# Optimization experiments

Measured on AMD Instinct MI355X. Metric: run time of the kernel, lower is better.

The kernel has to match this reference:

```python
import math
import jax, jax.numpy as jnp
import numpy as np

N_NODES = 100000
N_EDGES = 1600000
IN_DIM = 512
HID = 128
OUT_DIM = 1
N_LAYERS = 8
ALPHA = 0.1
THETA = 0.5


def setup_inputs() -> dict:
    key = jax.random.key(0)
    ks = jax.random.split(key, 8)
    x = jax.random.normal(ks[0], (N_NODES, IN_DIM), dtype=jnp.float32)
    edge_index = jax.random.randint(ks[1], (2, N_EDGES), 0, N_NODES, dtype=jnp.int64)
    edge_weight = jax.random.uniform(ks[2], (N_EDGES,), dtype=jnp.float32)
    s_in = 1.0 / math.sqrt(IN_DIM)
    s_h = 1.0 / math.sqrt(HID)
    W_in = jax.random.uniform(ks[3], (IN_DIM, HID), jnp.float32, -s_in, s_in)
    b_in = jax.random.uniform(ks[4], (HID,), jnp.float32, -s_in, s_in)
    W_layers = jax.random.uniform(ks[5], (N_LAYERS, HID, HID), jnp.float32, -s_h, s_h)
    W_out = jax.random.uniform(ks[6], (HID, OUT_DIM), jnp.float32, -s_h, s_h)
    b_out = jax.random.uniform(ks[7], (OUT_DIM,), jnp.float32, -s_h, s_h)
    return {"x": x, "edge_index": edge_index, "edge_weight": edge_weight,
            "W_in": W_in, "b_in": b_in, "W_layers": W_layers,
            "W_out": W_out, "b_out": b_out}


def _gcn_norm(edge_index, n_nodes, dtype):
    # gcn_norm with add_self_loops=True and unit edge weights
    # (GCN2Net never forwards edge_weight into GCN2Conv).
    loop = jnp.arange(n_nodes, dtype=edge_index.dtype)
    src = jnp.concatenate([edge_index[0], loop])
    dst = jnp.concatenate([edge_index[1], loop])
    w = jnp.ones(src.shape[0], dtype=dtype)
    deg = jax.ops.segment_sum(w, dst, num_segments=n_nodes)
    dinv = jnp.where(deg > 0, jax.lax.rsqrt(deg), 0.0).astype(dtype)
    norm = dinv[src] * w * dinv[dst]
    return src, dst, norm


def reference(x, edge_index, edge_weight, W_in, b_in, W_layers, W_out, b_out):
    n = x.shape[0]
    src, dst, norm = _gcn_norm(edge_index, n, x.dtype)

    x = x @ W_in + b_in          # initial_proj: [N, HID]
    x0 = x
    for i in range(N_LAYERS):
        # sparse neighbor aggregation: A_hat @ x
        agg = jax.ops.segment_sum(x[src] * norm[:, None], dst, num_segments=n)
        # initial residual
        h = (1.0 - ALPHA) * agg + ALPHA * x0
        # identity mapping (shared_weights=True): (1-beta)*h + beta*(h @ W)
        beta = math.log(THETA / (i + 1) + 1.0)
        x = (1.0 - beta) * h + beta * (h @ W_layers[i])
        x = jax.nn.relu(x)
        # dropout omitted (eval mode / drop_prob=0)
    return x @ W_out + b_out     # final_proj: [N, OUT_DIM]
```

## Files before the change

### kernel.cpp

```cpp
#include <hip/hip_runtime.h>
#include <math.h>

#define NN 100000
#define NE 1600000
#define IN_DIM 512
#define HID 128
#define N_LAYERS 8
#define NB 98
#define PADMAX 2000000
#define NBUCK 391
#define BCAP2 4608
#define EPB 4096

typedef __attribute__((ext_vector_type(4))) float f32x4;
typedef __attribute__((ext_vector_type(8))) _Float16 h16x8;
typedef __attribute__((ext_vector_type(2))) _Float16 h16x2;


__global__ __launch_bounds__(256) void bucket2_kernel(
    const int* __restrict__ src, const int* __restrict__ dst,
    int* __restrict__ deg, int* __restrict__ bcnt, int2* __restrict__ pairs) {
    __shared__ int hist[NBUCK];
    __shared__ int scan_[NBUCK + 1];
    __shared__ int gb[NBUCK];
    __shared__ int curs[NBUCK];
    __shared__ int2 lp[EPB];
    int t = threadIdx.x;
    int e0 = blockIdx.x * EPB;
    int ne = NE - e0; if (ne > EPB) ne = EPB;

    for (int i = t; i < NBUCK; i += 256) hist[i] = 0;
    __syncthreads();
    for (int i = t; i < ne; i += 256) {
        int d = dst[e0 + i];
        atomicAdd(&hist[d >> 8], 1);
        atomicAdd(&deg[d], 1);
    }
    __syncthreads();

    if (t < 64) {
        int run = 0;
        for (int c = 0; c < 7; ++c) {
            int i = c * 64 + t;
            int h = (i < NBUCK) ? hist[i] : 0;
            int v = h;
            for (int off = 1; off < 64; off <<= 1) {
                int tmp = __shfl_up(v, off, 64);
                if (t >= off) v += tmp;
            }
            if (i < NBUCK) scan_[i] = run + v - h;
            run += __shfl(v, 63, 64);
        }
        if (t == 0) scan_[NBUCK] = run;
    }
    __syncthreads();

    for (int i = t; i < NBUCK; i += 256) {
        int h = hist[i];
        gb[i] = h ? atomicAdd(&bcnt[i], h) : 0;
        curs[i] = scan_[i];
    }
    __syncthreads();

    for (int i = t; i < ne; i += 256) {
        int d = dst[e0 + i], s = src[e0 + i];
        int slot = atomicAdd(&curs[d >> 8], 1);
        lp[slot] = make_int2(s, d);
    }
    __syncthreads();

    for (int i = t; i < ne; i += 256) {
        int lo = 0, hi = NBUCK;
        while (hi - lo > 1) {
            int mid = (lo + hi) >> 1;
            if (scan_[mid] <= i) lo = mid; else hi = mid;
        }
        pairs[(size_t)lo * BCAP2 + gb[lo] + (i - scan_[lo])] = lp[i];
    }
}

__global__ void scan1_kernel(const int* __restrict__ deg, int* __restrict__ bsum) {
    __shared__ int s[16];
    int gi = blockIdx.x * 1024 + threadIdx.x;
    int d = (gi < NN) ? deg[gi] : 0;
    int r = (d + 3) & ~3;
    for (int off = 32; off; off >>= 1) r += __shfl_down(r, off, 64);
    if ((threadIdx.x & 63) == 0) s[threadIdx.x >> 6] = r;
    __syncthreads();
    if (threadIdx.x == 0) {
        int t = 0;
        for (int i = 0; i < 16; ++i) t += s[i];
        bsum[blockIdx.x] = t;
    }
}

__global__ void scan2_kernel(const int* __restrict__ bsum, int* __restrict__ boff,
                             int* __restrict__ row_ptr,
                             _Float16* __restrict__ sa, _Float16* __restrict__ sb) {
    __shared__ int s[128];
    int tid = threadIdx.x;
    sa[(size_t)NN * HID + tid] = (_Float16)0.f;
    sb[(size_t)NN * HID + tid] = (_Float16)0.f;
    int v = (tid < NB) ? bsum[tid] : 0;
    s[tid] = v;
    __syncthreads();
    for (int off = 1; off < 128; off <<= 1) {
        int t = (tid >= off) ? s[tid - off] : 0;
        __syncthreads();
        s[tid] += t;
        __syncthreads();
    }
    if (tid < NB) boff[tid] = s[tid] - v;
    if (tid == NB - 1) row_ptr[NN] = s[tid];
}

__global__ void scan3_kernel(const int* __restrict__ deg, const int* __restrict__ boff,
                             int* __restrict__ row_ptr, int* __restrict__ cursor,
                             float* __restrict__ dinv) {
    __shared__ int s[1024];
    int tid = threadIdx.x;
    int gi = blockIdx.x * 1024 + tid;
    int d = (gi < NN) ? deg[gi] : 0;
    int v = (d + 3) & ~3;
    s[tid] = v;
    __syncthreads();
    for (int off = 1; off < 1024; off <<= 1) {
        int t = (tid >= off) ? s[tid - off] : 0;
        __syncthreads();
        s[tid] += t;
        __syncthreads();
    }
    if (gi < NN) {
        int o = boff[blockIdx.x] + s[tid] - v;
        row_ptr[gi] = o;
        cursor[gi]  = o;
        dinv[gi]    = rsqrtf((float)(d + 1));
    }
}

__global__ __launch_bounds__(512) void fill2_kernel(
    const int* __restrict__ bcnt, const int2* __restrict__ pairs,
    const int* __restrict__ row_ptr, int* __restrict__ cursor,
    int* __restrict__ col) {
    int b = blockIdx.x;
    int n = bcnt[b];
    const int2* seg = pairs + (size_t)b * BCAP2;
#pragma unroll 4
    for (int i = threadIdx.x; i < n; i += 512) {
        int2 sd = seg[i];
        int pos = atomicAdd(&cursor[sd.y], 1);
        col[pos] = sd.x;
    }
    __syncthreads();
    int d0 = b * 256;
    int d1 = d0 + 256; if (d1 > NN) d1 = NN;
    for (int d = d0 + threadIdx.x; d < d1; d += 512) {
        int rp  = row_ptr[d];
        int end = cursor[d];
        int pend = rp + ((end - rp + 3) & ~3);
        for (int p = end; p < pend; ++p) col[p] = NN;
    }
}


__global__ void wprep_init_kernel(const float* __restrict__ W,
                                  _Float16* __restrict__ Bhi, _Float16* __restrict__ Blo) {
    int t = blockIdx.x * 256 + threadIdx.x;
    if (t >= 8 * 16 * 64) return;
    int lane = t & 63, nkk = t >> 6;
    int n = nkk >> 4, kk = nkk & 15;
    int scol = n * 16 + (lane & 15);
    int sr0 = kk * 32 + (lane >> 4) * 8;
#pragma unroll
    for (int j = 0; j < 8; ++j) {
        float w = W[(size_t)(sr0 + j) * HID + scol];
        _Float16 hi = (_Float16)w;
        _Float16 lo = (_Float16)(w - (float)hi);
        Bhi[(size_t)t * 8 + j] = hi;
        Blo[(size_t)t * 8 + j] = lo;
    }
}

__global__ void wprep_layers_kernel(const float* __restrict__ WL,
                                    _Float16* __restrict__ Bhi, _Float16* __restrict__ Blo) {
    int t = blockIdx.x * 256 + threadIdx.x;
    if (t >= N_LAYERS * 8 * 4 * 64) return;
    int layer = t >> 11;
    int r = t & 2047;
    int lane = r & 63, nkk = r >> 6;
    int n = nkk >> 2, kk = nkk & 3;
    const float* W = WL + (size_t)layer * HID * HID;
    int scol = n * 16 + (lane & 15);
    int sr0 = kk * 32 + (lane >> 4) * 8;
#pragma unroll
    for (int j = 0; j < 8; ++j) {
        float w = W[(size_t)(sr0 + j) * HID + scol];
        _Float16 hi = (_Float16)w;
        _Float16 lo = (_Float16)(w - (float)hi);
        Bhi[(size_t)t * 8 + j] = hi;
        Blo[(size_t)t * 8 + j] = lo;
    }
}


__device__ inline int xsw(int row, int blk) {
    return row * 512 + ((blk ^ (row & 7)) << 3);
}

__global__ __launch_bounds__(1024) void init_mfma_kernel(
    const float* __restrict__ x, const h16x8* __restrict__ Bhi, const h16x8* __restrict__ Blo,
    const float* __restrict__ b, const float* __restrict__ dinv,
    _Float16* __restrict__ ycur, _Float16* __restrict__ x0h) {
    __shared__ _Float16 xs[64 * 512];
    int t = threadIdx.x;
    int row0 = blockIdx.x * 64;

#pragma unroll
    for (int i = 0; i < 4; ++i) {
        int c = t + 1024 * i;
        int row = c >> 6, blk = c & 63;
        int grow = row0 + row; if (grow >= NN) grow = NN - 1;
        const float* p = x + (size_t)grow * IN_DIM + blk * 8;
        float4 v0 = *(const float4*)p;
        float4 v1 = *(const float4*)(p + 4);
        h16x8 h;
        h[0] = (_Float16)v0.x; h[1] = (_Float16)v0.y;
        h[2] = (_Float16)v0.z; h[3] = (_Float16)v0.w;
        h[4] = (_Float16)v1.x; h[5] = (_Float16)v1.y;
        h[6] = (_Float16)v1.z; h[7] = (_Float16)v1.w;
        *(h16x8*)&xs[xsw(row, blk)] = h;
    }
    __syncthreads();

    int lane = t & 63, wid = t >> 6;
    int nsel = wid & 7, mhalf = (wid >> 3) * 2;
    int rsel = lane & 15, ksel = lane >> 4;

    f32x4 acc[2];
#pragma unroll
    for (int m = 0; m < 2; ++m) acc[m] = (f32x4){0.f, 0.f, 0.f, 0.f};

#pragma unroll
    for (int kk = 0; kk < 16; ++kk) {
        h16x8 bh = Bhi[(nsel * 16 + kk) * 64 + lane];
        h16x8 bl = Blo[(nsel * 16 + kk) * 64 + lane];
#pragma unroll
        for (int m = 0; m < 2; ++m) {
            h16x8 a = *(const h16x8*)&xs[xsw((mhalf + m) * 16 + rsel, kk * 4 + ksel)];
            acc[m] = __builtin_amdgcn_mfma_f32_16x16x32_f16(a, bh, acc[m], 0, 0, 0);
            acc[m] = __builtin_amdgcn_mfma_f32_16x16x32_f16(a, bl, acc[m], 0, 0, 0);
        }
    }

    int col = nsel * 16 + rsel;
    float bias = b[col];
#pragma unroll
    for (int m = 0; m < 2; ++m) {
#pragma unroll
        for (int r = 0; r < 4; ++r) {
            int row = row0 + (mhalf + m) * 16 + ksel * 4 + r;
            if (row < NN) {
                float v = acc[m][r] + bias;
                float di = dinv[row];
                ycur[(size_t)row * HID + col] = (_Float16)(di * v);
                x0h[(size_t)row * HID + col]  = (_Float16)(0.1f * v);
            }
        }
    }
}


__device__ inline int hsw(int row, int blk) {
    return row * 128 + ((blk ^ (row & 7)) << 3);
}

__global__ __launch_bounds__(512) void fused_layer_kernel(
    const _Float16* __restrict__ y, const _Float16* __restrict__ x0,
    const int* __restrict__ row_ptr, const int* __restrict__ col,
    const float* __restrict__ dinv,
    const h16x8* __restrict__ Bhi, const h16x8* __restrict__ Blo,
    float beta, _Float16* __restrict__ yout) {
    __shared__ _Float16 hs[64 * 128];
    int t = threadIdx.x;
    int lane = t & 63, wid = t >> 6;
    int node0 = blockIdx.x * 64;
    int g = lane >> 4, q = lane & 15;

    h16x8 bh[4], bl[4];
#pragma unroll
    for (int kk = 0; kk < 4; ++kk) {
        bh[kk] = Bhi[(wid * 4 + kk) * 64 + lane];
        bl[kk] = Blo[(wid * 4 + kk) * 64 + lane];
    }

    const h16x8* x8 = (const h16x8*)y;
#pragma unroll
    for (int j = 0; j < 2; ++j) {
        int ln = wid * 8 + j * 4 + g;
        int node = node0 + ln;
        int valid = node < NN;
        int nd = valid ? node : 0;
        float di = dinv[nd];
        h16x8 sv = x8[(size_t)nd * 16 + q];
        h16x8 zv = ((const h16x8*)x0)[(size_t)nd * 16 + q];

        float acc[8];
#pragma unroll
        for (int jj = 0; jj < 8; ++jj) acc[jj] = 0.f;

        int p  = valid ? row_ptr[nd] : 0;
        int p1 = valid ? row_ptr[nd + 1] : 0;
#pragma unroll 2
        for (; p < p1; p += 4) {
            int4 c4 = *(const int4*)(col + p);
            h16x8 v0 = x8[(size_t)c4.x * 16 + q];
            h16x8 v1 = x8[(size_t)c4.y * 16 + q];
            h16x8 v2 = x8[(size_t)c4.z * 16 + q];
            h16x8 v3 = x8[(size_t)c4.w * 16 + q];
#pragma unroll
            for (int jj = 0; jj < 8; ++jj)
                acc[jj] += ((float)v0[jj] + (float)v1[jj])
                         + ((float)v2[jj] + (float)v3[jj]);
        }

        float d9 = 0.9f * di;
        h16x8 o16;
#pragma unroll
        for (int jj = 0; jj < 8; ++jj) {
            float s = acc[jj] + (float)sv[jj];
            o16[jj] = (_Float16)(d9 * s + (float)zv[jj]);
        }
        *(h16x8*)&hs[hsw(ln, q)] = o16;
    }
    __syncthreads();

    int rsel = lane & 15, ksel = lane >> 4;
    f32x4 acc[4];
#pragma unroll
    for (int m = 0; m < 4; ++m) acc[m] = (f32x4){0.f, 0.f, 0.f, 0.f};

#pragma unroll
    for (int m = 0; m < 4; ++m)
#pragma unroll
        for (int kk = 0; kk < 4; ++kk) {
            h16x8 a = *(const h16x8*)&hs[hsw(m * 16 + rsel, kk * 4 + ksel)];
            acc[m] = __builtin_amdgcn_mfma_f32_16x16x32_f16(a, bh[kk], acc[m], 0, 0, 0);
            acc[m] = __builtin_amdgcn_mfma_f32_16x16x32_f16(a, bl[kk], acc[m], 0, 0, 0);
        }

    float ob = 1.0f - beta;
    int colw = wid * 16 + rsel;
#pragma unroll
    for (int m = 0; m < 4; ++m) {
#pragma unroll
        for (int r = 0; r < 4; ++r) {
            int lr = m * 16 + ksel * 4 + r;
            int row = node0 + lr;
            if (row < NN) {
                float h = (float)hs[lr * 128 + (((colw >> 3) ^ (lr & 7)) << 3) + (colw & 7)];
                float v = ob * h + beta * acc[m][r];
                v = v > 0.f ? v : 0.f;
                yout[(size_t)row * HID + colw] = (_Float16)(dinv[row] * v);
            }
        }
    }
}


__global__ __launch_bounds__(256) void final16_kernel(
    const _Float16* __restrict__ y, const int* __restrict__ deg,
    const float* __restrict__ Wout, const float* __restrict__ bout,
    float* __restrict__ out) {
    int node = blockIdx.x * 4 + (threadIdx.x >> 6);
    int lane = threadIdx.x & 63;
    h16x2 a = ((const h16x2*)y)[(size_t)node * 64 + lane];
    float2 w = ((const float2*)Wout)[lane];
    float v = (float)a[0] * w.x + (float)a[1] * w.y;
#pragma unroll
    for (int off = 32; off; off >>= 1) v += __shfl_down(v, off, 64);
    if (lane == 0) out[node] = v * sqrtf((float)(deg[node] + 1)) + bout[0];
}


extern "C" void kernel_launch(void* const* d_in, const int* in_sizes, int n_in,
                              void* d_out, int out_size, void* d_ws, size_t ws_size,
                              hipStream_t stream) {
    const float* x_in     = (const float*)d_in[0];
    const int*   ei       = (const int*)d_in[1];
    const float* W_in     = (const float*)d_in[3];
    const float* b_in     = (const float*)d_in[4];
    const float* W_layers = (const float*)d_in[5];
    const float* W_out    = (const float*)d_in[6];
    const float* b_out    = (const float*)d_in[7];
    float* out = (float*)d_out;

    const int* src = ei;
    const int* dst = ei + NE;

    char* ws = (char*)d_ws;
    size_t off = 0;
    auto alloc = [&](size_t bytes) {
        size_t p = off;
        off = (off + bytes + 255) & ~(size_t)255;
        return p;
    };
    int*   deg     = (int*)(ws + alloc((size_t)NN * 4));
    int*   bcnt    = (int*)(ws + alloc((size_t)NBUCK * 4));
    float* dinv    = (float*)(ws + alloc((size_t)NN * 4));
    int*   row_ptr = (int*)(ws + alloc((size_t)(NN + 1) * 4));
    int*   cursor  = (int*)(ws + alloc((size_t)NN * 4));
    int*   bsum    = (int*)(ws + alloc((size_t)NB * 4));
    int*   boff    = (int*)(ws + alloc((size_t)NB * 4));
    int*   col     = (int*)(ws + alloc((size_t)PADMAX * 4));
    size_t x0_off  = alloc((size_t)NN * HID * 2);
    _Float16* x0h  = (_Float16*)(ws + x0_off);
    int2*  pairs   = (int2*)(ws + x0_off);
    _Float16* bufA = (_Float16*)(ws + alloc((size_t)(NN + 16) * HID * 2));
    _Float16* bufB = (_Float16*)(ws + alloc((size_t)(NN + 16) * HID * 2));
    _Float16* Bhi0 = (_Float16*)(ws + alloc((size_t)IN_DIM * HID * 2));
    _Float16* Blo0 = (_Float16*)(ws + alloc((size_t)IN_DIM * HID * 2));
    _Float16* BhiL = (_Float16*)(ws + alloc((size_t)N_LAYERS * HID * HID * 2));
    _Float16* BloL = (_Float16*)(ws + alloc((size_t)N_LAYERS * HID * HID * 2));

    hipMemsetAsync(deg, 0, (size_t)((char*)bcnt - (char*)deg) + (size_t)NBUCK * 4, stream);

    bucket2_kernel<<<(NE + EPB - 1) / EPB, 256, 0, stream>>>(src, dst, deg, bcnt, pairs);
    scan1_kernel<<<NB, 1024, 0, stream>>>(deg, bsum);
    scan2_kernel<<<1, 128, 0, stream>>>(bsum, boff, row_ptr, bufA, bufB);
    scan3_kernel<<<NB, 1024, 0, stream>>>(deg, boff, row_ptr, cursor, dinv);
    fill2_kernel<<<NBUCK, 512, 0, stream>>>(bcnt, pairs, row_ptr, cursor, col);

    wprep_init_kernel<<<32, 256, 0, stream>>>(W_in, Bhi0, Blo0);
    wprep_layers_kernel<<<64, 256, 0, stream>>>(W_layers, BhiL, BloL);

    init_mfma_kernel<<<(NN + 63) / 64, 1024, 0, stream>>>(
        x_in, (const h16x8*)Bhi0, (const h16x8*)Blo0, b_in, dinv, bufA, x0h);

    _Float16* cur = bufA;
    _Float16* nxt = bufB;
    for (int l = 0; l < N_LAYERS; ++l) {
        float beta = logf(0.5f / (float)(l + 1) + 1.0f);
        fused_layer_kernel<<<(NN + 63) / 64, 512, 0, stream>>>(
            cur, x0h, row_ptr, col, dinv,
            (const h16x8*)(BhiL + (size_t)l * HID * HID),
            (const h16x8*)(BloL + (size_t)l * HID * HID), beta, nxt);
        _Float16* tmp = cur; cur = nxt; nxt = tmp;
    }

    final16_kernel<<<NN / 4, 256, 0, stream>>>(cur, deg, W_out, b_out, out);
}
```

Before: 897.6 us.

## Fuse final projection into last layer, pack edge pairs, shrink init blocks

Several changes at once. The final output projection is fused into the last layer kernel through a template flag, which removes the fp16 store and re-read of the last activations. Edge (src, dst-offset) pairs are packed into one int, and the CSR fill uses shared-memory cursors instead of global atomics on a cursor array. The two weight-prep kernels are merged into one launch, and the init GEMM uses 32-row, 512-thread blocks with no bounds checks. The bounds removal relies on NN being divisible by 32, and packing assumes node ids fit in 17 bits.

```diff
diff --git a/kernel.cpp b/kernel.cpp
--- a/kernel.cpp
+++ b/kernel.cpp
@@ -19,12 +19,12 @@
 
 __global__ __launch_bounds__(256) void bucket2_kernel(
     const int* __restrict__ src, const int* __restrict__ dst,
-    int* __restrict__ deg, int* __restrict__ bcnt, int2* __restrict__ pairs) {
+    int* __restrict__ deg, int* __restrict__ bcnt, int* __restrict__ pairs) {
     __shared__ int hist[NBUCK];
     __shared__ int scan_[NBUCK + 1];
     __shared__ int gb[NBUCK];
     __shared__ int curs[NBUCK];
-    __shared__ int2 lp[EPB];
+    __shared__ int lp[EPB];
     int t = threadIdx.x;
     int e0 = blockIdx.x * EPB;
     int ne = NE - e0; if (ne > EPB) ne = EPB;
@@ -65,7 +65,7 @@
     for (int i = t; i < ne; i += 256) {
         int d = dst[e0 + i], s = src[e0 + i];
         int slot = atomicAdd(&curs[d >> 8], 1);
-        lp[slot] = make_int2(s, d);
+        lp[slot] = ((d & 255) << 17) | s;
     }
     __syncthreads();
 
@@ -115,8 +115,7 @@
 }
 
 __global__ void scan3_kernel(const int* __restrict__ deg, const int* __restrict__ boff,
-                             int* __restrict__ row_ptr, int* __restrict__ cursor,
-                             float* __restrict__ dinv) {
+                             int* __restrict__ row_ptr, float* __restrict__ dinv) {
     __shared__ int s[1024];
     int tid = threadIdx.x;
     int gi = blockIdx.x * 1024 + tid;
@@ -131,74 +130,78 @@
         __syncthreads();
     }
     if (gi < NN) {
-        int o = boff[blockIdx.x] + s[tid] - v;
-        row_ptr[gi] = o;
-        cursor[gi]  = o;
+        row_ptr[gi] = boff[blockIdx.x] + s[tid] - v;
         dinv[gi]    = rsqrtf((float)(d + 1));
     }
 }
 
 __global__ __launch_bounds__(512) void fill2_kernel(
-    const int* __restrict__ bcnt, const int2* __restrict__ pairs,
-    const int* __restrict__ row_ptr, int* __restrict__ cursor,
-    int* __restrict__ col) {
+    const int* __restrict__ bcnt, const int* __restrict__ pairs,
+    const int* __restrict__ row_ptr, int* __restrict__ col) {
+    __shared__ int lcur[256];
     int b = blockIdx.x;
+    int d0 = b * 256;
+    for (int i = threadIdx.x; i < 256; i += 512) {
+        int d = d0 + i;
+        lcur[i] = (d < NN) ? row_ptr[d] : 0;
+    }
+    __syncthreads();
     int n = bcnt[b];
-    const int2* seg = pairs + (size_t)b * BCAP2;
+    const int* seg = pairs + (size_t)b * BCAP2;
 #pragma unroll 4
     for (int i = threadIdx.x; i < n; i += 512) {
-        int2 sd = seg[i];
-        int pos = atomicAdd(&cursor[sd.y], 1);
-        col[pos] = sd.x;
-    }
-    __syncthreads();
-    int d0 = b * 256;
-    int d1 = d0 + 256; if (d1 > NN) d1 = NN;
-    for (int d = d0 + threadIdx.x; d < d1; d += 512) {
-        int rp  = row_ptr[d];
-        int end = cursor[d];
-        int pend = rp + ((end - rp + 3) & ~3);
-        for (int p = end; p < pend; ++p) col[p] = NN;
-    }
-}
-
-
-__global__ void wprep_init_kernel(const float* __restrict__ W,
-                                  _Float16* __restrict__ Bhi, _Float16* __restrict__ Blo) {
-    int t = blockIdx.x * 256 + threadIdx.x;
-    if (t >= 8 * 16 * 64) return;
-    int lane = t & 63, nkk = t >> 6;
-    int n = nkk >> 4, kk = nkk & 15;
-    int scol = n * 16 + (lane & 15);
-    int sr0 = kk * 32 + (lane >> 4) * 8;
-#pragma unroll
-    for (int j = 0; j < 8; ++j) {
-        float w = W[(size_t)(sr0 + j) * HID + scol];
-        _Float16 hi = (_Float16)w;
-        _Float16 lo = (_Float16)(w - (float)hi);
-        Bhi[(size_t)t * 8 + j] = hi;
-        Blo[(size_t)t * 8 + j] = lo;
-    }
-}
-
-__global__ void wprep_layers_kernel(const float* __restrict__ WL,
-                                    _Float16* __restrict__ Bhi, _Float16* __restrict__ Blo) {
-    int t = blockIdx.x * 256 + threadIdx.x;
-    if (t >= N_LAYERS * 8 * 4 * 64) return;
-    int layer = t >> 11;
-    int r = t & 2047;
-    int lane = r & 63, nkk = r >> 6;
-    int n = nkk >> 2, kk = nkk & 3;
-    const float* W = WL + (size_t)layer * HID * HID;
-    int scol = n * 16 + (lane & 15);
-    int sr0 = kk * 32 + (lane >> 4) * 8;
-#pragma unroll
-    for (int j = 0; j < 8; ++j) {
-        float w = W[(size_t)(sr0 + j) * HID + scol];
-        _Float16 hi = (_Float16)w;
-        _Float16 lo = (_Float16)(w - (float)hi);
-        Bhi[(size_t)t * 8 + j] = hi;
-        Blo[(size_t)t * 8 + j] = lo;
+        int v = seg[i];
+        int pos = atomicAdd(&lcur[v >> 17], 1);
+        col[pos] = v & 0x1FFFF;
+    }
+    __syncthreads();
+    for (int i = threadIdx.x; i < 256; i += 512) {
+        int d = d0 + i;
+        if (d < NN) {
+            int rp = row_ptr[d];
+            int end = lcur[i];
+            int pend = rp + ((end - rp + 3) & ~3);
+            for (int p = end; p < pend; ++p) col[p] = NN;
+        }
+    }
+}
+
+
+__global__ void wprep_kernel(const float* __restrict__ W_in, const float* __restrict__ WL,
+                             _Float16* __restrict__ Bhi0, _Float16* __restrict__ Blo0,
+                             _Float16* __restrict__ BhiL, _Float16* __restrict__ BloL) {
+    int bid = blockIdx.x;
+    if (bid < 32) {
+        int t = bid * 256 + threadIdx.x;
+        int lane = t & 63, nkk = t >> 6;
+        int n = nkk >> 4, kk = nkk & 15;
+        int scol = n * 16 + (lane & 15);
+        int sr0 = kk * 32 + (lane >> 4) * 8;
+#pragma unroll
+        for (int j = 0; j < 8; ++j) {
+            float w = W_in[(size_t)(sr0 + j) * HID + scol];
+            _Float16 hi = (_Float16)w;
+            _Float16 lo = (_Float16)(w - (float)hi);
+            Bhi0[(size_t)t * 8 + j] = hi;
+            Blo0[(size_t)t * 8 + j] = lo;
+        }
+    } else {
+        int t = (bid - 32) * 256 + threadIdx.x;
+        int layer = t >> 11;
+        int r = t & 2047;
+        int lane = r & 63, nkk = r >> 6;
+        int n = nkk >> 2, kk = nkk & 3;
+        const float* W = WL + (size_t)layer * HID * HID;
+        int scol = n * 16 + (lane & 15);
+        int sr0 = kk * 32 + (lane >> 4) * 8;
+#pragma unroll
+        for (int j = 0; j < 8; ++j) {
+            float w = W[(size_t)(sr0 + j) * HID + scol];
+            _Float16 hi = (_Float16)w;
+            _Float16 lo = (_Float16)(w - (float)hi);
+            BhiL[(size_t)t * 8 + j] = hi;
+            BloL[(size_t)t * 8 + j] = lo;
+        }
     }
 }
 
@@ -207,20 +210,19 @@
     return row * 512 + ((blk ^ (row & 7)) << 3);
 }
 
-__global__ __launch_bounds__(1024) void init_mfma_kernel(
+__global__ __launch_bounds__(512) void init_mfma_kernel(
     const float* __restrict__ x, const h16x8* __restrict__ Bhi, const h16x8* __restrict__ Blo,
     const float* __restrict__ b, const float* __restrict__ dinv,
     _Float16* __restrict__ ycur, _Float16* __restrict__ x0h) {
-    __shared__ _Float16 xs[64 * 512];
+    __shared__ _Float16 xs[32 * 512];
     int t = threadIdx.x;
-    int row0 = blockIdx.x * 64;
+    int row0 = blockIdx.x * 32;
 
 #pragma unroll
     for (int i = 0; i < 4; ++i) {
-        int c = t + 1024 * i;
+        int c = t + 512 * i;
         int row = c >> 6, blk = c & 63;
-        int grow = row0 + row; if (grow >= NN) grow = NN - 1;
-        const float* p = x + (size_t)grow * IN_DIM + blk * 8;
+        const float* p = x + (size_t)(row0 + row) * IN_DIM + blk * 8;
         float4 v0 = *(const float4*)p;
         float4 v1 = *(const float4*)(p + 4);
         h16x8 h;
@@ -233,7 +235,6 @@
     __syncthreads();
 
     int lane = t & 63, wid = t >> 6;
-    int nsel = wid & 7, mhalf = (wid >> 3) * 2;
     int rsel = lane & 15, ksel = lane >> 4;
 
     f32x4 acc[2];
@@ -242,29 +243,27 @@
 
 #pragma unroll
     for (int kk = 0; kk < 16; ++kk) {
-        h16x8 bh = Bhi[(nsel * 16 + kk) * 64 + lane];
-        h16x8 bl = Blo[(nsel * 16 + kk) * 64 + lane];
+        h16x8 bh = Bhi[(wid * 16 + kk) * 64 + lane];
+        h16x8 bl = Blo[(wid * 16 + kk) * 64 + lane];
 #pragma unroll
         for (int m = 0; m < 2; ++m) {
-            h16x8 a = *(const h16x8*)&xs[xsw((mhalf + m) * 16 + rsel, kk * 4 + ksel)];
+            h16x8 a = *(const h16x8*)&xs[xsw(m * 16 + rsel, kk * 4 + ksel)];
             acc[m] = __builtin_amdgcn_mfma_f32_16x16x32_f16(a, bh, acc[m], 0, 0, 0);
             acc[m] = __builtin_amdgcn_mfma_f32_16x16x32_f16(a, bl, acc[m], 0, 0, 0);
         }
     }
 
-    int col = nsel * 16 + rsel;
+    int col = wid * 16 + rsel;
     float bias = b[col];
 #pragma unroll
     for (int m = 0; m < 2; ++m) {
 #pragma unroll
         for (int r = 0; r < 4; ++r) {
-            int row = row0 + (mhalf + m) * 16 + ksel * 4 + r;
-            if (row < NN) {
-                float v = acc[m][r] + bias;
-                float di = dinv[row];
-                ycur[(size_t)row * HID + col] = (_Float16)(di * v);
-                x0h[(size_t)row * HID + col]  = (_Float16)(0.1f * v);
-            }
+            int row = row0 + m * 16 + ksel * 4 + r;
+            float v = acc[m][r] + bias;
+            float di = dinv[row];
+            ycur[(size_t)row * HID + col] = (_Float16)(di * v);
+            x0h[(size_t)row * HID + col]  = (_Float16)(0.1f * v);
         }
     }
 }
@@ -274,12 +273,15 @@
     return row * 128 + ((blk ^ (row & 7)) << 3);
 }
 
+template <int LAST>
 __global__ __launch_bounds__(512) void fused_layer_kernel(
     const _Float16* __restrict__ y, const _Float16* __restrict__ x0,
     const int* __restrict__ row_ptr, const int* __restrict__ col,
     const float* __restrict__ dinv,
     const h16x8* __restrict__ Bhi, const h16x8* __restrict__ Blo,
-    float beta, _Float16* __restrict__ yout) {
+    float beta, _Float16* __restrict__ yout,
+    const float* __restrict__ Wout, const float* __restrict__ bout,
+    float* __restrict__ out) {
     __shared__ _Float16 hs[64 * 128];
     int t = threadIdx.x;
     int lane = t & 63, wid = t >> 6;
@@ -350,35 +352,52 @@
 
     float ob = 1.0f - beta;
     int colw = wid * 16 + rsel;
-#pragma unroll
-    for (int m = 0; m < 4; ++m) {
-#pragma unroll
-        for (int r = 0; r < 4; ++r) {
-            int lr = m * 16 + ksel * 4 + r;
-            int row = node0 + lr;
-            if (row < NN) {
+
+    if constexpr (!LAST) {
+#pragma unroll
+        for (int m = 0; m < 4; ++m) {
+#pragma unroll
+            for (int r = 0; r < 4; ++r) {
+                int lr = m * 16 + ksel * 4 + r;
+                int row = node0 + lr;
+                if (row < NN) {
+                    float h = (float)hs[lr * 128 + (((colw >> 3) ^ (lr & 7)) << 3) + (colw & 7)];
+                    float v = ob * h + beta * acc[m][r];
+                    v = v > 0.f ? v : 0.f;
+                    yout[(size_t)row * HID + colw] = (_Float16)(dinv[row] * v);
+                }
+            }
+        }
+    } else {
+        __shared__ float red[64][9];
+        float wv = Wout[colw];
+#pragma unroll
+        for (int m = 0; m < 4; ++m) {
+#pragma unroll
+            for (int r = 0; r < 4; ++r) {
+                int lr = m * 16 + ksel * 4 + r;
                 float h = (float)hs[lr * 128 + (((colw >> 3) ^ (lr & 7)) << 3) + (colw & 7)];
                 float v = ob * h + beta * acc[m][r];
                 v = v > 0.f ? v : 0.f;
-                yout[(size_t)row * HID + colw] = (_Float16)(dinv[row] * v);
+                float pp = v * wv;
+                pp += __shfl_xor(pp, 1, 64);
+                pp += __shfl_xor(pp, 2, 64);
+                pp += __shfl_xor(pp, 4, 64);
+                pp += __shfl_xor(pp, 8, 64);
+                if (rsel == 0) red[lr][wid] = pp;
             }
         }
-    }
-}
-
-
-__global__ __launch_bounds__(256) void final16_kernel(
-    const _Float16* __restrict__ y, const int* __restrict__ deg,
-    const float* __restrict__ Wout, const float* __restrict__ bout,
-    float* __restrict__ out) {
-    int node = blockIdx.x * 4 + (threadIdx.x >> 6);
-    int lane = threadIdx.x & 63;
-    h16x2 a = ((const h16x2*)y)[(size_t)node * 64 + lane];
-    float2 w = ((const float2*)Wout)[lane];
-    float v = (float)a[0] * w.x + (float)a[1] * w.y;
-#pragma unroll
-    for (int off = 32; off; off >>= 1) v += __shfl_down(v, off, 64);
-    if (lane == 0) out[node] = v * sqrtf((float)(deg[node] + 1)) + bout[0];
+        __syncthreads();
+        if (t < 64) {
+            int row = node0 + t;
+            if (row < NN) {
+                float s = bout[0];
+#pragma unroll
+                for (int w = 0; w < 8; ++w) s += red[t][w];
+                out[row] = s;
+            }
+        }
+    }
 }
 
 
@@ -408,13 +427,12 @@
     int*   bcnt    = (int*)(ws + alloc((size_t)NBUCK * 4));
     float* dinv    = (float*)(ws + alloc((size_t)NN * 4));
     int*   row_ptr = (int*)(ws + alloc((size_t)(NN + 1) * 4));
-    int*   cursor  = (int*)(ws + alloc((size_t)NN * 4));
     int*   bsum    = (int*)(ws + alloc((size_t)NB * 4));
     int*   boff    = (int*)(ws + alloc((size_t)NB * 4));
     int*   col     = (int*)(ws + alloc((size_t)PADMAX * 4));
     size_t x0_off  = alloc((size_t)NN * HID * 2);
     _Float16* x0h  = (_Float16*)(ws + x0_off);
-    int2*  pairs   = (int2*)(ws + x0_off);
+    int*   pairs   = (int*)(ws + x0_off);
     _Float16* bufA = (_Float16*)(ws + alloc((size_t)(NN + 16) * HID * 2));
     _Float16* bufB = (_Float16*)(ws + alloc((size_t)(NN + 16) * HID * 2));
     _Float16* Bhi0 = (_Float16*)(ws + alloc((size_t)IN_DIM * HID * 2));
@@ -427,25 +445,31 @@
     bucket2_kernel<<<(NE + EPB - 1) / EPB, 256, 0, stream>>>(src, dst, deg, bcnt, pairs);
     scan1_kernel<<<NB, 1024, 0, stream>>>(deg, bsum);
     scan2_kernel<<<1, 128, 0, stream>>>(bsum, boff, row_ptr, bufA, bufB);
-    scan3_kernel<<<NB, 1024, 0, stream>>>(deg, boff, row_ptr, cursor, dinv);
-    fill2_kernel<<<NBUCK, 512, 0, stream>>>(bcnt, pairs, row_ptr, cursor, col);
-
-    wprep_init_kernel<<<32, 256, 0, stream>>>(W_in, Bhi0, Blo0);
-    wprep_layers_kernel<<<64, 256, 0, stream>>>(W_layers, BhiL, BloL);
-
-    init_mfma_kernel<<<(NN + 63) / 64, 1024, 0, stream>>>(
+    scan3_kernel<<<NB, 1024, 0, stream>>>(deg, boff, row_ptr, dinv);
+    fill2_kernel<<<NBUCK, 512, 0, stream>>>(bcnt, pairs, row_ptr, col);
+
+    wprep_kernel<<<96, 256, 0, stream>>>(W_in, W_layers, Bhi0, Blo0, BhiL, BloL);
+
+    init_mfma_kernel<<<NN / 32, 512, 0, stream>>>(
         x_in, (const h16x8*)Bhi0, (const h16x8*)Blo0, b_in, dinv, bufA, x0h);
 
     _Float16* cur = bufA;
     _Float16* nxt = bufB;
-    for (int l = 0; l < N_LAYERS; ++l) {
+    for (int l = 0; l < N_LAYERS - 1; ++l) {
         float beta = logf(0.5f / (float)(l + 1) + 1.0f);
-        fused_layer_kernel<<<(NN + 63) / 64, 512, 0, stream>>>(
+        fused_layer_kernel<0><<<(NN + 63) / 64, 512, 0, stream>>>(
             cur, x0h, row_ptr, col, dinv,
             (const h16x8*)(BhiL + (size_t)l * HID * HID),
-            (const h16x8*)(BloL + (size_t)l * HID * HID), beta, nxt);
+            (const h16x8*)(BloL + (size_t)l * HID * HID), beta, nxt,
+            nullptr, nullptr, nullptr);
         _Float16* tmp = cur; cur = nxt; nxt = tmp;
     }
-
-    final16_kernel<<<NN / 4, 256, 0, stream>>>(cur, deg, W_out, b_out, out);
-}
+    {
+        float beta = logf(0.5f / (float)N_LAYERS + 1.0f);
+        fused_layer_kernel<1><<<(NN + 63) / 64, 512, 0, stream>>>(
+            cur, x0h, row_ptr, col, dinv,
+            (const h16x8*)(BhiL + (size_t)(N_LAYERS - 1) * HID * HID),
+            (const h16x8*)(BloL + (size_t)(N_LAYERS - 1) * HID * HID), beta, nxt,
+            W_out, b_out, out);
+    }
+}
```

Measured after the change: 850.0 us. 1.06x faster.
